# Kernel tuning notes

Measured on AMD Instinct MI355X. Metric: run time of the kernel, lower is better.

Reference implementation:

```python
import jax, jax.numpy as jnp
import numpy as np

NTYPES = 4
RCUT = 6.0
MIXED_TYPES = False
BOX = 40.0  # Angstrom, sets realistic atomic density


def setup_inputs() -> dict:
    key = jax.random.key(0)
    k1, k2 = jax.random.split(key)
    nframes, nloc = 2, 4096
    coord = jax.random.uniform(k1, (nframes, nloc * 3), dtype=jnp.float32) * BOX
    atype = jax.random.randint(k2, (nframes, nloc), 0, NTYPES, dtype=jnp.int32)
    return {"coord": coord, "atype": atype}


def reference(coord, atype):
    # cell=None branch: extended coords == local coords, nall == nloc
    nframes = coord.shape[0]
    c = coord.reshape(nframes, -1, 3)              # (f, nloc, 3)
    nloc = c.shape[1]
    # diff[f, i, j] = coord[j] - coord[i], shape (f, nloc, nall, 3)
    diff = c[:, None, :, :] - c[:, :, None, :]
    rr2 = jnp.sum(diff * diff, axis=-1)            # (f, nloc, nall)
    # mask self-pairs with inf (torch sets diff rows to inf before squaring)
    eye = jnp.eye(nloc, dtype=bool)
    rr2 = jnp.where(eye[None, :, :], jnp.inf, rr2)
    min_rr2 = jnp.min(rr2, axis=-1)                # (f, nloc)
    mask = rr2 < RCUT ** 2                         # (f, nloc, nall)
    if not MIXED_TYPES:
        # per-type neighbor counts via one-hot contraction (replaces the
        # Python loop over ntypes in the torch code; same math)
        onehot = jax.nn.one_hot(atype, NTYPES, dtype=jnp.int32)  # (f, nall, t)
        nnei = jnp.einsum('fij,fjt->fit', mask.astype(jnp.int32), onehot)
    else:
        valid = (atype >= 0)[:, None, :]
        nnei = jnp.sum(mask & valid, axis=-1).astype(jnp.int32)[..., None]
    max_nnei = jnp.max(nnei, axis=1)               # (f, ntypes) or (f, 1)
    return min_rr2, max_nnei
```

## Files before the change

kernel.cpp:

```cpp
#include <hip/hip_runtime.h>
#include <stdint.h>

#define NFRAMES 2
#define NT 4
#define BLK 256
#define NJ 64
#define IPT 4
#define FBLK 128

__device__ __forceinline__ float bcast_f(float v, int l) {
    return __uint_as_float(__builtin_amdgcn_readlane(__float_as_uint(v), l));
}

template <bool SELFCHK>
__device__ __forceinline__ void do_pair(float cx, float cy, float cz, unsigned sval,
                                        int j, int i,
                                        float xi, float yi, float zi,
                                        float& mm, unsigned& cc) {
#pragma clang fp contract(off)
    float dx = cx - xi;
    float dy = cy - yi;
    float dz = cz - zi;
    float xx = dx * dx;
    float yy = dy * dy;
    float zz = dz * dz;
    float r2 = (xx + yy) + zz;
    bool self = SELFCHK && (j == i);
    mm = fminf(mm, self ? __builtin_inff() : r2);
    bool near = (r2 < 36.0f) && !self;
    cc += near ? sval : 0u;
}

template <bool SELFCHK>
__device__ __forceinline__ void chunk_loop(float bx, float by, float bz, unsigned bs,
                                           int jbase,
                                           const int (&ii)[IPT],
                                           const float (&xi)[IPT],
                                           const float (&yi)[IPT],
                                           const float (&zi)[IPT],
                                           float (&mA)[IPT], float (&mB)[IPT],
                                           unsigned (&cA)[IPT], unsigned (&cB)[IPT]) {
#pragma unroll 8
    for (int l = 0; l < 64; l += 2) {
        float cx0 = bcast_f(bx, l), cy0 = bcast_f(by, l), cz0 = bcast_f(bz, l);
        unsigned s0 = __builtin_amdgcn_readlane(bs, l);
        const int j0 = jbase + l;
#pragma unroll
        for (int k = 0; k < IPT; ++k)
            do_pair<SELFCHK>(cx0, cy0, cz0, s0, j0, ii[k], xi[k], yi[k], zi[k], mA[k], cA[k]);
        float cx1 = bcast_f(bx, l + 1), cy1 = bcast_f(by, l + 1), cz1 = bcast_f(bz, l + 1);
        unsigned s1 = __builtin_amdgcn_readlane(bs, l + 1);
#pragma unroll
        for (int k = 0; k < IPT; ++k)
            do_pair<SELFCHK>(cx1, cy1, cz1, s1, j0 + 1, ii[k], xi[k], yi[k], zi[k], mB[k], cB[k]);
    }
}

__global__ __launch_bounds__(BLK) void ns_pair_kernel(const float* __restrict__ coord,
                                                      const int* __restrict__ atype,
                                                      uint2* __restrict__ part,
                                                      float* __restrict__ out,
                                                      int nloc) {
    const int f = blockIdx.z;
    const int q = nloc / IPT;
    const int ib = blockIdx.y * BLK;
    const int jbase = blockIdx.x * (nloc / NJ);

    if (blockIdx.x == 0 && blockIdx.y == 0 && f == 0 && threadIdx.x < NFRAMES * NT)
        ((unsigned*)out)[(size_t)NFRAMES * nloc + threadIdx.x] = 0u;

    const float* cf = coord + (size_t)f * nloc * 3;
    const int*   tf = atype + (size_t)f * nloc;

    const int lane = threadIdx.x & 63;
    const int jl = jbase + lane;
    const float bx = cf[3 * jl], by = cf[3 * jl + 1], bz = cf[3 * jl + 2];
    const unsigned bs = 1u << (tf[jl] * 8);

    int ii[IPT];
    float xi[IPT], yi[IPT], zi[IPT];
    float mA[IPT], mB[IPT];
    unsigned cA[IPT], cB[IPT];
    bool ov = false;
#pragma unroll
    for (int k = 0; k < IPT; ++k) {
        const int base = ib + k * q;
        ii[k] = base + threadIdx.x;
        xi[k] = cf[3 * ii[k]];
        yi[k] = cf[3 * ii[k] + 1];
        zi[k] = cf[3 * ii[k] + 2];
        mA[k] = mB[k] = __builtin_inff();
        cA[k] = cB[k] = 0u;
        ov |= (jbase >= base) && (jbase < base + BLK);
    }

    if (ov)
        chunk_loop<true >(bx, by, bz, bs, jbase, ii, xi, yi, zi, mA, mB, cA, cB);
    else
        chunk_loop<false>(bx, by, bz, bs, jbase, ii, xi, yi, zi, mA, mB, cA, cB);

    const size_t pb = ((size_t)blockIdx.x * NFRAMES + f) * nloc;
#pragma unroll
    for (int k = 0; k < IPT; ++k)
        part[pb + ii[k]] = make_uint2(__float_as_uint(fminf(mA[k], mB[k])), cA[k] + cB[k]);
}

__global__ __launch_bounds__(FBLK) void ns_finalize_kernel(const uint2* __restrict__ part,
                                                           float* __restrict__ out,
                                                           int nloc) {
    const int nbpf = nloc / FBLK;
    const int f = blockIdx.x / nbpf;
    const int i = (blockIdx.x % nbpf) * FBLK + threadIdx.x;

    float ma = __builtin_inff(), mb = __builtin_inff();
    unsigned cacc = 0u, cbacc = 0u;
#pragma unroll 8
    for (int jb = 0; jb < NJ; jb += 2) {
        uint2 va = part[((size_t)jb * NFRAMES + f) * nloc + i];
        uint2 vb = part[((size_t)(jb + 1) * NFRAMES + f) * nloc + i];
        ma = fminf(ma, __uint_as_float(va.x));
        mb = fminf(mb, __uint_as_float(vb.x));
        cacc += va.y;
        cbacc += vb.y;
    }
    out[(size_t)f * nloc + i] = fminf(ma, mb);
    const unsigned c = cacc + cbacc;

    int m0 = (int)(c & 255u);
    int m1 = (int)((c >> 8) & 255u);
    int m2 = (int)((c >> 16) & 255u);
    int m3 = (int)(c >> 24);
    for (int off = 32; off > 0; off >>= 1) {
        m0 = max(m0, __shfl_xor(m0, off, 64));
        m1 = max(m1, __shfl_xor(m1, off, 64));
        m2 = max(m2, __shfl_xor(m2, off, 64));
        m3 = max(m3, __shfl_xor(m3, off, 64));
    }
    __shared__ int red[FBLK / 64][NT];
    const int wid = threadIdx.x >> 6;
    if ((threadIdx.x & 63) == 0) {
        red[wid][0] = m0; red[wid][1] = m1; red[wid][2] = m2; red[wid][3] = m3;
    }
    __syncthreads();
    if (threadIdx.x < NT) {
        const int t = threadIdx.x;
        const int m = max(red[0][t], red[1][t]);
        atomicMax((unsigned*)out + (size_t)NFRAMES * nloc + f * NT + t,
                  __float_as_uint((float)m));
    }
}

extern "C" void kernel_launch(void* const* d_in, const int* in_sizes, int n_in,
                              void* d_out, int out_size, void* d_ws, size_t ws_size,
                              hipStream_t stream) {
    const float* coord = (const float*)d_in[0];
    const int*   atype = (const int*)d_in[1];
    const int nloc = in_sizes[1] / NFRAMES;

    float* out  = (float*)d_out;
    uint2* part = (uint2*)d_ws;

    dim3 grid(NJ, nloc / (BLK * IPT), NFRAMES);
    ns_pair_kernel<<<grid, dim3(BLK), 0, stream>>>(coord, atype, part, out, nloc);

    const int nbpf = nloc / FBLK;
    ns_finalize_kernel<<<NFRAMES * nbpf, FBLK, 0, stream>>>(part, out, nloc);
}
```

Before: 24.21 us.

## Stage j-tile in LDS, halve i-per-thread, and use single-wave finalize blocks

The pair kernel now loads each 64-atom j tile into shared memory as float4 (x, y, z, packed type bit). It reads these back as broadcast LDS loads instead of taking them from per-lane registers with readlane. Each thread now handles 2 i-atoms instead of 4, which doubles the number of blocks to spread work across more CUs, at the cost of reusing each j value across fewer i. The finalize kernel drops to one 64-thread wave per block, which removes the shared-memory reduction and barrier but doubles the number of atomicMax calls. The trade-offs are the LDS read latency and the __syncthreads against better occupancy and less cross-lane traffic.

```diff
diff --git a/kernel.cpp b/kernel.cpp
--- a/kernel.cpp
+++ b/kernel.cpp
@@ -5,12 +5,9 @@
 #define NT 4
 #define BLK 256
 #define NJ 64
-#define IPT 4
-#define FBLK 128
-
-__device__ __forceinline__ float bcast_f(float v, int l) {
-    return __uint_as_float(__builtin_amdgcn_readlane(__float_as_uint(v), l));
-}
+#define JT 64
+#define IPT 2
+#define FBLK 64
 
 template <bool SELFCHK>
 __device__ __forceinline__ void do_pair(float cx, float cy, float cz, unsigned sval,
@@ -32,27 +29,26 @@
 }
 
 template <bool SELFCHK>
-__device__ __forceinline__ void chunk_loop(float bx, float by, float bz, unsigned bs,
-                                           int jbase,
-                                           const int (&ii)[IPT],
-                                           const float (&xi)[IPT],
-                                           const float (&yi)[IPT],
-                                           const float (&zi)[IPT],
-                                           float (&mA)[IPT], float (&mB)[IPT],
-                                           unsigned (&cA)[IPT], unsigned (&cB)[IPT]) {
+__device__ __forceinline__ void tile_loop(const float4* __restrict__ sj, int jbase,
+                                          const int (&ii)[IPT],
+                                          const float (&xi)[IPT],
+                                          const float (&yi)[IPT],
+                                          const float (&zi)[IPT],
+                                          float (&mA)[IPT], float (&mB)[IPT],
+                                          unsigned (&cA)[IPT], unsigned (&cB)[IPT]) {
 #pragma unroll 8
-    for (int l = 0; l < 64; l += 2) {
-        float cx0 = bcast_f(bx, l), cy0 = bcast_f(by, l), cz0 = bcast_f(bz, l);
-        unsigned s0 = __builtin_amdgcn_readlane(bs, l);
+    for (int l = 0; l < JT; l += 2) {
+        float4 c0 = sj[l];
+        float4 c1 = sj[l + 1];
+        const unsigned s0 = __float_as_uint(c0.w);
+        const unsigned s1 = __float_as_uint(c1.w);
         const int j0 = jbase + l;
 #pragma unroll
         for (int k = 0; k < IPT; ++k)
-            do_pair<SELFCHK>(cx0, cy0, cz0, s0, j0, ii[k], xi[k], yi[k], zi[k], mA[k], cA[k]);
-        float cx1 = bcast_f(bx, l + 1), cy1 = bcast_f(by, l + 1), cz1 = bcast_f(bz, l + 1);
-        unsigned s1 = __builtin_amdgcn_readlane(bs, l + 1);
+            do_pair<SELFCHK>(c0.x, c0.y, c0.z, s0, j0, ii[k], xi[k], yi[k], zi[k], mA[k], cA[k]);
 #pragma unroll
         for (int k = 0; k < IPT; ++k)
-            do_pair<SELFCHK>(cx1, cy1, cz1, s1, j0 + 1, ii[k], xi[k], yi[k], zi[k], mB[k], cB[k]);
+            do_pair<SELFCHK>(c1.x, c1.y, c1.z, s1, j0 + 1, ii[k], xi[k], yi[k], zi[k], mB[k], cB[k]);
     }
 }
 
@@ -64,7 +60,7 @@
     const int f = blockIdx.z;
     const int q = nloc / IPT;
     const int ib = blockIdx.y * BLK;
-    const int jbase = blockIdx.x * (nloc / NJ);
+    const int jbase = blockIdx.x * JT;
 
     if (blockIdx.x == 0 && blockIdx.y == 0 && f == 0 && threadIdx.x < NFRAMES * NT)
         ((unsigned*)out)[(size_t)NFRAMES * nloc + threadIdx.x] = 0u;
@@ -72,10 +68,13 @@
     const float* cf = coord + (size_t)f * nloc * 3;
     const int*   tf = atype + (size_t)f * nloc;
 
-    const int lane = threadIdx.x & 63;
-    const int jl = jbase + lane;
-    const float bx = cf[3 * jl], by = cf[3 * jl + 1], bz = cf[3 * jl + 2];
-    const unsigned bs = 1u << (tf[jl] * 8);
+    __shared__ float4 sj[JT];
+    if (threadIdx.x < JT) {
+        const int jl = jbase + threadIdx.x;
+        sj[threadIdx.x] = make_float4(cf[3 * jl], cf[3 * jl + 1], cf[3 * jl + 2],
+                                      __uint_as_float(1u << (tf[jl] * 8)));
+    }
+    __syncthreads();
 
     int ii[IPT];
     float xi[IPT], yi[IPT], zi[IPT];
@@ -95,9 +94,9 @@
     }
 
     if (ov)
-        chunk_loop<true >(bx, by, bz, bs, jbase, ii, xi, yi, zi, mA, mB, cA, cB);
+        tile_loop<true >(sj, jbase, ii, xi, yi, zi, mA, mB, cA, cB);
     else
-        chunk_loop<false>(bx, by, bz, bs, jbase, ii, xi, yi, zi, mA, mB, cA, cB);
+        tile_loop<false>(sj, jbase, ii, xi, yi, zi, mA, mB, cA, cB);
 
     const size_t pb = ((size_t)blockIdx.x * NFRAMES + f) * nloc;
 #pragma unroll
@@ -114,7 +113,7 @@
 
     float ma = __builtin_inff(), mb = __builtin_inff();
     unsigned cacc = 0u, cbacc = 0u;
-#pragma unroll 8
+#pragma unroll 16
     for (int jb = 0; jb < NJ; jb += 2) {
         uint2 va = part[((size_t)jb * NFRAMES + f) * nloc + i];
         uint2 vb = part[((size_t)(jb + 1) * NFRAMES + f) * nloc + i];
@@ -136,17 +135,11 @@
         m2 = max(m2, __shfl_xor(m2, off, 64));
         m3 = max(m3, __shfl_xor(m3, off, 64));
     }
-    __shared__ int red[FBLK / 64][NT];
-    const int wid = threadIdx.x >> 6;
-    if ((threadIdx.x & 63) == 0) {
-        red[wid][0] = m0; red[wid][1] = m1; red[wid][2] = m2; red[wid][3] = m3;
-    }
-    __syncthreads();
     if (threadIdx.x < NT) {
         const int t = threadIdx.x;
-        const int m = max(red[0][t], red[1][t]);
+        const int mv = (t == 0) ? m0 : (t == 1) ? m1 : (t == 2) ? m2 : m3;
         atomicMax((unsigned*)out + (size_t)NFRAMES * nloc + f * NT + t,
-                  __float_as_uint((float)m));
+                  __float_as_uint((float)mv));
     }
 }
 
```

After: 24.89 us. 1.03x slower.
